# Kernel optimization log

Hardware: AMD Instinct MI355X
Metric: run time of the kernel (lower is better)

Reference implementation:

```python
import jax, jax.numpy as jnp
import numpy as np
from jax import lax

M = 384   # latent_seq_length (match states); insert states = M+1; K = 2M+1
A = 21    # alphabet_length
B = 64    # batch
L = 256   # max observed sequence length
NEG = -1.0e32  # pyro uses -1/epsilon with epsilon=1e-32 for impossible transitions


def _state_indices(Mloc):
    # state k = m + M*g: match states (g=0) m in 0..M-1, insert states (g=1) m in 0..M
    m_k = np.concatenate([np.arange(Mloc), np.arange(Mloc + 1)]).astype(np.int32)
    g_k = np.concatenate([np.zeros(Mloc, np.int32), np.ones(Mloc + 1, np.int32)])
    s_k = (m_k + 1 - g_k).astype(np.int32)  # next decision position, in 0..M
    return m_k, g_k, s_k


def _arrange(precursor_seq_logits, insert_seq_logits, insert_logits, delete_logits):
    """Profile(M) state arranger: assemble initial/transition/emission logits of the
    MuE profile HMM from insertion (r) and deletion (u) log-simplex params.
    insert_logits[m,j] = [log(1-r_mj), log(r_mj)], same for delete/u. Boundary
    convention r_M=1, u_M=0. Vectorized (gathers + cumsum of the delete chain)
    instead of pyro's dense (M,3,2,K,K) transfer einsum -- same math."""
    Mloc = precursor_seq_logits.shape[0]
    dt = precursor_seq_logits.dtype
    m_k, g_k, s_k = _state_indices(Mloc)
    pad_r = jnp.tile(jnp.array([[[NEG, 0.0]]], dt), (1, 3, 1))  # r_M = 1
    pad_u = jnp.tile(jnp.array([[[0.0, NEG]]], dt), (1, 3, 1))  # u_M = 0
    lre = jnp.concatenate([insert_logits, pad_r], 0)  # (M+1,3,2)
    lue = jnp.concatenate([delete_logits, pad_u], 0)  # (M+1,3,2)
    # delete-chain log prob per skipped position j (enter-and-leave delete, type j=2)
    d2 = insert_logits[:, 2, 0] + delete_logits[:, 2, 1]  # (M,)
    C = jnp.concatenate([jnp.zeros((1,), dt), jnp.cumsum(d2), jnp.zeros((1,), dt)])  # C[j]=sum_{i<j} d2[i]
    # per-source-state factors (K,)
    src_stay = lre[s_k, g_k, 0]   # log(1-r_{s,g})
    src_del = lue[s_k, g_k, 1]    # log u_{s,g}
    src_match = lue[s_k, g_k, 0]  # log(1-u_{s,g})
    src_ins = lre[s_k, g_k, 1]    # log r_{s,g}
    # per-target-state factors (K,)
    t_match = lre[m_k, 2, 0] + lue[m_k, 2, 0]
    t_ins = lre[m_k, 2, 1]
    is_ins = g_k == 1
    t_term = jnp.where(is_ins, t_ins, t_match)
    # transition matrix (K,K): direct step, delete-chain step, or impossible
    chain = (src_stay + src_del - C[s_k + 1])[:, None] + C[m_k][None, :]
    same = m_k[None, :] == s_k[:, None]
    fwdm = m_k[None, :] > s_k[:, None]
    direct = jnp.where(is_ins[None, :], src_ins[:, None], (src_stay + src_match)[:, None])
    trans = jnp.where(same, direct, jnp.where(fwdm, chain + t_term[None, :], NEG))
    # initial vector: virtual source (m=-1, g=0) -> s=0 with j=0 params
    i_direct = jnp.where(is_ins, lre[0, 0, 1], lre[0, 0, 0] + lue[0, 0, 0])
    i_chain = lre[0, 0, 0] + lue[0, 0, 1] - C[1] + C[m_k]
    init = jnp.where(m_k == 0, i_direct, i_chain + t_term)
    # emission logits: match states emit precursor, insert states emit insert_seq
    obs = jnp.concatenate([precursor_seq_logits, insert_seq_logits], 0)  # (K,A)
    return init, trans, obs


def _forward(precursor_seq, insert_seq, insert, delete, seq_data, local_scale):
    # log-softmax normalizations done in ProfileHMM.model
    p = precursor_seq - jax.nn.logsumexp(precursor_seq, -1, keepdims=True)
    iseq = insert_seq - jax.nn.logsumexp(insert_seq, -1, keepdims=True)
    r = insert - jax.nn.logsumexp(insert, -1, keepdims=True)
    u = delete - jax.nn.logsumexp(delete, -1, keepdims=True)
    init, trans, obs = _arrange(p, iseq, r, u)
    # MissingDataDiscreteHMM normalizes all logits
    init = init - jax.nn.logsumexp(init)
    trans = trans - jax.nn.logsumexp(trans, -1, keepdims=True)
    obs = obs - jax.nn.logsumexp(obs, -1, keepdims=True)
    # per-position per-state emission log-prob; all-zero rows (missing) give 0
    vl = jnp.einsum('bla,ka->blk', seq_data, obs)  # (B,L,K)
    alpha = init[None, :] + vl[:, 0]               # (B,K)
    Tprob = jnp.exp(trans)                         # (K,K)

    def step(a, vlt):
        # logsumexp_k(a[b,k] + trans[k,kp]) via stable exp-matmul-log
        mx = jnp.max(a, -1, keepdims=True)
        pr = jnp.exp(a - mx) @ Tprob
        return jnp.log(jnp.maximum(pr, 1e-30)) + mx + vlt, None

    alpha, _ = lax.scan(step, alpha, jnp.moveaxis(vl[:, 1:], 1, 0))
    return local_scale[0] * jax.nn.logsumexp(alpha, -1)  # (B,) scaled log-probs


def setup_inputs() -> dict:
    key = jax.random.key(0)
    ks = jax.random.split(key, 6)
    precursor_seq = jax.random.normal(ks[0], (M, A), jnp.float32)
    insert_seq = jax.random.normal(ks[1], (M + 1, A), jnp.float32)
    indel_prior = jnp.array([10.0, 0.0], jnp.float32)  # indel_prior_bias=10 -> rare indels
    insert = indel_prior + jax.random.normal(ks[2], (M, 3, 2), jnp.float32)
    delete = indel_prior + jax.random.normal(ks[3], (M, 3, 2), jnp.float32)
    lengths = jax.random.randint(ks[4], (B,), L // 2, L + 1)
    letters = jax.random.randint(ks[5], (B, L), 0, A)
    onehot = jax.nn.one_hot(letters, A, dtype=jnp.float32)
    mask = (jnp.arange(L)[None, :] < lengths[:, None]).astype(jnp.float32)
    seq_data = onehot * mask[:, :, None]  # zero rows past length = missing data
    return {"precursor_seq": precursor_seq, "insert_seq": insert_seq,
            "insert": insert, "delete": delete, "seq_data": seq_data,
            "local_scale": jnp.ones((1,), jnp.float32)}


def reference(precursor_seq, insert_seq, insert, delete, seq_data, local_scale):
    return _forward(precursor_seq, insert_seq, insert, delete, seq_data, local_scale)
```

## Files before the change

### kernel.cpp

```cpp
#include <hip/hip_runtime.h>


#define NEGC (-1.0e32f)

typedef float v2f __attribute__((ext_vector_type(2)));

#if __has_builtin(__builtin_elementwise_fma)
#define VFMA(a,b,c) __builtin_elementwise_fma((a),(b),(c))
#else
static __device__ __forceinline__ v2f VFMA(v2f a, v2f b, v2f c) {
    v2f r; r.x = fmaf(a.x,b.x,c.x); r.y = fmaf(a.y,b.y,c.y); return r;
}
#endif
#if __has_builtin(__builtin_elementwise_max)
#define VMAX(a,b) __builtin_elementwise_max((a),(b))
#else
static __device__ __forceinline__ v2f VMAX(v2f a, v2f b) {
    v2f r; r.x = fmaxf(a.x,b.x); r.y = fmaxf(a.y,b.y); return r;
}
#endif
static __device__ __forceinline__ v2f mkv2(float a, float b) { v2f r; r.x = a; r.y = b; return r; }

template<int CTRL>
__device__ __forceinline__ float fdpp(float x) {
    union { float f; int i; } u, r;
    u.f = x;
    r.i = __builtin_amdgcn_update_dpp(0, u.i, CTRL, 0xF, 0xF, true);
    return r.f;
}
__device__ __forceinline__ float wsr1(float x) { return fdpp<0x138>(x); }
__device__ __forceinline__ float rdlane63(float x) {
    union { float f; int i; } u; u.f = x;
    u.i = __builtin_amdgcn_readlane(u.i, 63);
    return u.f;
}

#define L_TAB   0
#define L_ES    16128
#define L_LETS  16152
#define L_TOTAL 16224

#define S_RN    0
#define S_UN    2304
#define S_EWS   4608
#define S_ETMM  4993
#define S_ETII  5378
#define S_CS    5763
#define S_QA    6148
#define S_D2    6533
#define S_AEM   6917
#define S_AEI   7302
#define S_DMA   7687
#define S_DMB   8072
#define S_DIA   8457
#define S_DIB   8842
#define S_RAW   9227
#define S_RED   9998

struct Buf { v2f em0, em1, em2, ei0, ei1, ei2; float es; };

#define RENORM do { \
    v2f mv_ = VMAX(VMAX(Pm0,Pm1), VMAX(Pm2, VMAX(Pi0, VMAX(Pi1,Pi2)))); \
    float mxr_ = fmaxf(fmaxf(mv_.x, mv_.y), pi384); \
    mxr_ = fmaxf(mxr_, fdpp<0x111>(mxr_)); \
    mxr_ = fmaxf(mxr_, fdpp<0x112>(mxr_)); \
    mxr_ = fmaxf(mxr_, fdpp<0x114>(mxr_)); \
    mxr_ = fmaxf(mxr_, fdpp<0x118>(mxr_)); \
    mxr_ = fmaxf(mxr_, fdpp<0x142>(mxr_)); \
    mxr_ = fmaxf(mxr_, fdpp<0x143>(mxr_)); \
    float g_ = rdlane63(mxr_); \
    if (g_ > 0.f) { \
        float sc_ = 0x1p60f / g_; \
        logoff += __logf(g_) - 41.588830833596718565f; \
        Pm0 *= sc_; Pm1 *= sc_; Pm2 *= sc_; Pi0 *= sc_; Pi1 *= sc_; Pi2 *= sc_; pi384 *= sc_; \
    } \
} while (0)

#define FILL(LM, E) do { \
    int lmv_ = (LM); \
    int lmc_ = lmv_ > 20 ? 20 : lmv_; \
    const float* bp_ = smem + lmc_*768 + lane12; \
    float4 q0_ = ((const float4*)bp_)[0], q1_ = ((const float4*)bp_)[1], q2_ = ((const float4*)bp_)[2]; \
    E.em0 = mkv2(q0_.x,q0_.y); E.em1 = mkv2(q0_.z,q0_.w); E.em2 = mkv2(q1_.x,q1_.y); \
    E.ei0 = mkv2(q1_.z,q1_.w); E.ei1 = mkv2(q2_.x,q2_.y); E.ei2 = mkv2(q2_.z,q2_.w); \
    E.es = smem[L_ES + lmv_]; \
} while (0)

#define CORE(CUR, FAST) do { \
    float apx_ = wsr1(Pm2.y); \
    float oldPm_ = Pm2.y; \
    v2f Ap0_ = mkv2(apx_, Pm0.x), Ap1_ = mkv2(Pm0.y, Pm1.x), Ap2_ = mkv2(Pm1.y, Pm2.x); \
    v2f E0_ = VFMA(Pi0, Cei0, Ap0_*Cem0); \
    v2f E1_ = VFMA(Pi1, Cei1, Ap1_*Cem1); \
    v2f E2_ = VFMA(Pi2, Cei2, Ap2_*Cem2); \
    float i0_ = E0_.x; \
    float i1_ = fmaf(w1, i0_, E0_.y); \
    float i2_ = fmaf(w2, i1_, E1_.x); \
    float i3_ = fmaf(w3, i2_, E1_.y); \
    float i4_ = fmaf(w4, i3_, E2_.x); \
    float i5_ = fmaf(w5, i4_, E2_.y); \
    float bb_; \
    if (FAST) { bb_ = fmaf(Ar0, wsr1(i5_), i5_); } \
    else { \
        bb_ = i5_; \
        bb_ = fmaf(Ar0, fdpp<0x111>(bb_), bb_); \
        bb_ = fmaf(Ar1, fdpp<0x112>(bb_), bb_); \
        bb_ = fmaf(Ar2, fdpp<0x114>(bb_), bb_); \
        bb_ = fmaf(Ar3, fdpp<0x118>(bb_), bb_); \
        bb_ = fmaf(A15, fdpp<0x142>(bb_), bb_); \
        bb_ = fmaf(A31, fdpp<0x143>(bb_), bb_); \
    } \
    float bx_ = wsr1(bb_); \
    v2f Rv0_ = mkv2(bx_, fmaf(pw1, bx_, i0_)); \
    v2f Rv1_ = mkv2(fmaf(pw2, bx_, i1_), fmaf(pw3, bx_, i2_)); \
    v2f Rv2_ = mkv2(fmaf(pw4, bx_, i3_), fmaf(pw5, bx_, i4_)); \
    v2f nm0_ = VFMA(Cgm0, Rv0_, VFMA(Pi0, Cdmb0, Ap0_*Cdma0)); \
    v2f nm1_ = VFMA(Cgm1, Rv1_, VFMA(Pi1, Cdmb1, Ap1_*Cdma1)); \
    v2f nm2_ = VFMA(Cgm2, Rv2_, VFMA(Pi2, Cdmb2, Ap2_*Cdma2)); \
    v2f ni0_ = VFMA(Cgi0, Rv0_, VFMA(Pi0, Cdib0, Ap0_*Cdia0)); \
    v2f ni1_ = VFMA(Cgi1, Rv1_, VFMA(Pi1, Cdib1, Ap1_*Cdia1)); \
    v2f ni2_ = VFMA(Cgi2, Rv2_, VFMA(Pi2, Cdib2, Ap2_*Cdia2)); \
    float np_ = ((oldPm_ + pi384) + bb_) * CUR.es;  \
    Pm0 = nm0_*CUR.em0; Pm1 = nm1_*CUR.em1; Pm2 = nm2_*CUR.em2; \
    Pi0 = ni0_*CUR.ei0; Pi1 = ni1_*CUR.ei1; Pi2 = ni2_*CUR.ei2; \
    pi384 = np_; \
} while (0)

#define ITER(BA,BB,BC,LA,LB,LC,TIDX,FAST) do { \
    FILL(LA, BC); \
    LA = (int)lets[(TIDX)+5]; \
    CORE(BA, FAST); \
} while (0)

#define SCANLOOP(FAST) do { \
    for (int it = 0; it < bodies; ++it, t += 6) { \
        ITER(bA,bB,bC,lA,lB,lC,t,FAST); \
        ITER(bB,bC,bA,lB,lC,lA,t+1,FAST); \
        ITER(bC,bA,bB,lC,lA,lB,t+2,FAST); \
        ITER(bA,bB,bC,lA,lB,lC,t+3,FAST); \
        ITER(bB,bC,bA,lB,lC,lA,t+4,FAST); \
        ITER(bC,bA,bB,lC,lA,lB,t+5,FAST); \
        RENORM; \
    } \
    if (rem > 0) { ITER(bA,bB,bC,lA,lB,lC,t,FAST); ++t; } \
    if (rem > 1) { ITER(bB,bC,bA,lB,lC,lA,t,FAST); ++t; } \
    if (rem > 2) { ITER(bC,bA,bB,lC,lA,lB,t,FAST); ++t; } \
    if (rem > 3) { ITER(bA,bB,bC,lA,lB,lC,t,FAST); ++t; } \
    if (rem > 4) { ITER(bB,bC,bA,lB,lC,lA,t,FAST); ++t; } \
} while (0)

__global__ __launch_bounds__(256, 1) void hmm_fused(
    const float* __restrict__ ps, const float* __restrict__ iseq,
    const float* __restrict__ rr, const float* __restrict__ uu,
    const float* __restrict__ seq, const float* __restrict__ lsc,
    float* __restrict__ out)
{
    __shared__ float smem[L_TOTAL];
    const int tid = threadIdx.x;
    const int lane = tid & 63;
    const int wvid = tid >> 6;
    const int b = blockIdx.x;
    unsigned char* lets = (unsigned char*)(smem + L_LETS);

    float* rn   = smem + S_RN;
    float* un   = smem + S_UN;
    float* ews  = smem + S_EWS;
    float* etmm = smem + S_ETMM;
    float* etii = smem + S_ETII;
    float* Cs   = smem + S_CS;
    float* qa   = smem + S_QA;
    float* d2s  = smem + S_D2;
    float* cAEM = smem + S_AEM;
    float* cAEI = smem + S_AEI;
    float* cDMA = smem + S_DMA;
    float* cDMB = smem + S_DMB;
    float* cDIA = smem + S_DIA;
    float* cDIB = smem + S_DIB;
    float* rawv = smem + S_RAW;
    float* red  = smem + S_RED;

    {
        const float* p = seq + (size_t)b*5376 + tid*21;
        float s = 0.f, wsum = 0.f;
        #pragma unroll
        for (int a = 0; a < 21; ++a) { float v = p[a]; s += v; wsum += v*(float)a; }
        lets[tid] = (s > 0.5f) ? (unsigned char)(int)(wsum + 0.5f) : (unsigned char)21;
        if (tid < 8) lets[256 + tid] = (unsigned char)21;
    }
    for (int row = tid; row < 1152; row += 256) {
        float a = rr[row*2], c = rr[row*2+1];
        float mx = fmaxf(a, c);
        float l = mx + __logf(__expf(a-mx) + __expf(c-mx));
        rn[row*2] = a - l; rn[row*2+1] = c - l;
        a = uu[row*2]; c = uu[row*2+1];
        mx = fmaxf(a, c);
        l = mx + __logf(__expf(a-mx) + __expf(c-mx));
        un[row*2] = a - l; un[row*2+1] = c - l;
    }
    __syncthreads();
    for (int m = tid; m < 384; m += 256) {
        float d = rn[(m*3+2)*2+0] + un[(m*3+2)*2+1];
        d2s[m] = d;
        ews[m] = __expf(d);
        etmm[m] = __expf(rn[(m*3+2)*2+0] + un[(m*3+2)*2+0]);
        etii[m] = __expf(rn[(m*3+2)*2+1]);
    }
    if (tid == 0) { ews[384] = 0.f; etmm[384] = 0.f; etii[384] = 1.f; }
    __syncthreads();
    if (tid < 64) {
        float incl[6]; float z = 0.f;
        #pragma unroll
        for (int i = 0; i < 6; ++i) { z += d2s[lane*6+i]; incl[i] = z; }
        float tot = z;
        #pragma unroll
        for (int d = 1; d < 64; d <<= 1) { float q = __shfl_up(tot, d); if (lane >= d) tot += q; }
        float excl = __shfl_up(tot, 1); if (lane == 0) excl = 0.f;
        #pragma unroll
        for (int i = 0; i < 6; ++i) Cs[lane*6+i+1] = excl + incl[i];
        if (lane == 0) Cs[0] = 0.f;
    } else if (tid < 128) {
        float wv6[6], xv[6], incl[6];
        #pragma unroll
        for (int i = 0; i < 6; ++i) {
            int s = 384 - (lane*6 + i);
            wv6[i] = ews[s]; xv[i] = etii[s] + etmm[s];
        }
        float z = 0.f, Wl = 1.f;
        #pragma unroll
        for (int i = 0; i < 6; ++i) { z = fmaf(wv6[i], z, xv[i]); incl[i] = z; Wl *= wv6[i]; }
        float val = z, wt = Wl;
        #pragma unroll
        for (int d = 1; d < 64; d <<= 1) {
            float pv = __shfl_up(val, d); float pwv = __shfl_up(wt, d);
            if (lane >= d) { val = fmaf(wt, pv, val); wt *= pwv; }
        }
        float excl = __shfl_up(val, 1); if (lane == 0) excl = 0.f;
        float pp = 1.f;
        #pragma unroll
        for (int i = 0; i < 6; ++i) {
            pp *= wv6[i];
            qa[383 - (lane*6 + i)] = fmaf(excl, pp, incl[i]);
        }
        if (lane == 0) qa[384] = 0.f;
    }
    __syncthreads();
    for (int k = tid; k < 769; k += 256) {
        int g = (k < 384) ? 0 : 1;
        int m = (k < 384) ? k : (k - 384);
        int s = m + 1 - g;
        float ss, sd, smv, si;
        if (s <= 383) {
            int base = (s*3 + g)*2;
            ss = rn[base+0]; si = rn[base+1];
            smv = un[base+0]; sd = un[base+1];
        } else { ss = NEGC; si = 0.f; smv = 0.f; sd = NEGC; }
        float d0 = (s <= 383) ? (ss + smv) : NEGC;
        float d1 = si;
        float q = qa[s];
        float lq = (q > 0.f) ? __logf(q) : -1.0e30f;
        float ch = ss + sd + lq;
        float mx = fmaxf(fmaxf(d0, d1), ch);
        float Z = mx + __logf(__expf(d0-mx) + __expf(d1-mx) + __expf(ch-mx));
        float we = __expf(ss + sd - Z);
        float w0 = __expf(d0 - Z);
        float w1v = __expf(d1 - Z);
        if (g == 0) { cAEM[s] = we; cDMA[s] = w0; cDIA[s] = w1v; }
        else        { cAEI[s] = we; cDMB[s] = w0; cDIB[s] = w1v; }
    }
    if (tid == 0) { cAEM[0] = 0.f; cDMA[0] = 0.f; cDIA[0] = 0.f; }
    {
        float r000 = rn[0], r001 = rn[1];
        float u000 = un[0], u001 = un[1];
        for (int k = tid; k < 769; k += 256) {
            int g = (k < 384) ? 0 : 1;
            int m = (k < 384) ? k : (k - 384);
            float v;
            if (m == 0) v = g ? r001 : (r000 + u000);
            else {
                float tt = g ? ((m <= 383) ? rn[(m*3+2)*2+1] : 0.f)
                             : (rn[(m*3+2)*2+0] + un[(m*3+2)*2+0]);
                v = r000 + u001 - Cs[1] + Cs[m] + tt;
            }
            rawv[k] = v;
        }
    }
    __syncthreads();
    {
        float lmax = -3.0e38f;
        for (int k = tid; k < 769; k += 256) lmax = fmaxf(lmax, rawv[k]);
        #pragma unroll
        for (int d = 1; d < 64; d <<= 1) lmax = fmaxf(lmax, __shfl_xor(lmax, d));
        if (lane == 0) red[wvid] = lmax;
    }
    __syncthreads();
    {
        float gmax = fmaxf(fmaxf(red[0], red[1]), fmaxf(red[2], red[3]));
        float lsum = 0.f;
        for (int k = tid; k < 769; k += 256) lsum += __expf(rawv[k] - gmax);
        #pragma unroll
        for (int d = 1; d < 64; d <<= 1) lsum += __shfl_xor(lsum, d);
        if (lane == 0) red[4 + wvid] = lsum;
        __syncthreads();
        float lse = gmax + __logf(red[4] + red[5] + red[6] + red[7]);
        for (int k = tid; k < 769; k += 256) rawv[k] = __expf(rawv[k] - lse);
    }
    __syncthreads();
    const int j0 = lane*6;
    const int lane12 = lane*12;
    v2f Cem0=mkv2(cAEM[j0],cAEM[j0+1]), Cem1=mkv2(cAEM[j0+2],cAEM[j0+3]), Cem2=mkv2(cAEM[j0+4],cAEM[j0+5]);
    v2f Cei0=mkv2(cAEI[j0],cAEI[j0+1]), Cei1=mkv2(cAEI[j0+2],cAEI[j0+3]), Cei2=mkv2(cAEI[j0+4],cAEI[j0+5]);
    v2f Cdma0=mkv2(cDMA[j0],cDMA[j0+1]), Cdma1=mkv2(cDMA[j0+2],cDMA[j0+3]), Cdma2=mkv2(cDMA[j0+4],cDMA[j0+5]);
    v2f Cdmb0=mkv2(cDMB[j0],cDMB[j0+1]), Cdmb1=mkv2(cDMB[j0+2],cDMB[j0+3]), Cdmb2=mkv2(cDMB[j0+4],cDMB[j0+5]);
    v2f Cdia0=mkv2(cDIA[j0],cDIA[j0+1]), Cdia1=mkv2(cDIA[j0+2],cDIA[j0+3]), Cdia2=mkv2(cDIA[j0+4],cDIA[j0+5]);
    v2f Cdib0=mkv2(cDIB[j0],cDIB[j0+1]), Cdib1=mkv2(cDIB[j0+2],cDIB[j0+3]), Cdib2=mkv2(cDIB[j0+4],cDIB[j0+5]);
    v2f Cgm0=mkv2(etmm[j0],etmm[j0+1]), Cgm1=mkv2(etmm[j0+2],etmm[j0+3]), Cgm2=mkv2(etmm[j0+4],etmm[j0+5]);
    v2f Cgi0=mkv2(etii[j0],etii[j0+1]), Cgi1=mkv2(etii[j0+2],etii[j0+3]), Cgi2=mkv2(etii[j0+4],etii[j0+5]);
    v2f Pm0=mkv2(rawv[j0],rawv[j0+1]), Pm1=mkv2(rawv[j0+2],rawv[j0+3]), Pm2=mkv2(rawv[j0+4],rawv[j0+5]);
    v2f Pi0=mkv2(rawv[384+j0],rawv[384+j0+1]), Pi1=mkv2(rawv[384+j0+2],rawv[384+j0+3]), Pi2=mkv2(rawv[384+j0+4],rawv[384+j0+5]);
    float pi384 = rawv[768];
    const float W0=ews[j0], w1=ews[j0+1], w2=ews[j0+2], w3=ews[j0+3], w4=ews[j0+4], w5=ews[j0+5];
    __syncthreads();
    for (int row = tid; row < 769; row += 256) {
        const float* src = (row < 384) ? (ps + row*21) : (iseq + (row-384)*21);
        float mx = -3.0e38f;
        for (int a = 0; a < 21; ++a) mx = fmaxf(mx, src[a]);
        float sm2 = 0.f;
        for (int a = 0; a < 21; ++a) sm2 += __expf(src[a]-mx);
        float inv = 1.0f / sm2;
        if (row < 768) {
            int j = (row < 384) ? row : (row - 384);
            int slot = (j/6)*12 + ((row < 384) ? 0 : 6) + (j%6);
            float* dst = smem + L_TAB + slot;
            for (int a = 0; a < 21; ++a) dst[a*768] = __expf(src[a]-mx)*inv;
        } else {
            for (int a = 0; a < 21; ++a) smem[L_ES + a] = __expf(src[a]-mx)*inv;
            smem[L_ES + 21] = 1.0f; smem[L_ES + 22] = 1.0f; smem[L_ES + 23] = 1.0f;
        }
    }
    __syncthreads();
    if (wvid != 0) return;

    int n = 0;
    #pragma unroll
    for (int c = 0; c < 4; ++c)
        n += __popcll(__ballot(lets[c*64 + lane] != (unsigned char)21));

    const float pw1 = W0, pw2 = pw1*w1, pw3 = pw2*w2, pw4 = pw3*w3, pw5 = pw4*w4;
    const float W = pw5*w5;
    float p_ = W;
    const float Ar0 = p_;
    { float q = __shfl_up(p_, 1); p_ *= q; } const float Ar1 = p_;
    { float q = __shfl_up(p_, 2); p_ *= q; } const float Ar2 = p_;
    { float q = __shfl_up(p_, 4); p_ *= q; } const float Ar3 = p_;
    float prefR = W;
    #pragma unroll
    for (int d = 1; d < 16; d <<= 1) { float q = __shfl_up(prefR, d); if ((lane & 15) >= d) prefR *= q; }
    const int rw = lane >> 4;
    const float A15 = (rw == 1 || rw == 3) ? prefR : 0.f;
    const float s47 = __shfl(prefR, 47);
    const float A31 = (rw == 2) ? prefR : ((rw == 3) ? prefR * s47 : 0.f);
    bool bad = (Ar1 != 0.f) || (Ar2 != 0.f) || (Ar3 != 0.f)
             || ((A15 != 0.f) && ((lane & 15) >= 1))
             || ((A31 != 0.f) && (lane >= 33));
    const bool fastAll = (__ballot(bad) == 0ull);

    float logoff = 0.f;
    {
        int lm0 = (int)lets[0];
        const float* bp = smem + lm0*768 + lane12;
        float4 q0 = ((const float4*)bp)[0], q1 = ((const float4*)bp)[1], q2 = ((const float4*)bp)[2];
        Pm0 *= mkv2(q0.x,q0.y); Pm1 *= mkv2(q0.z,q0.w); Pm2 *= mkv2(q1.x,q1.y);
        Pi0 *= mkv2(q1.z,q1.w); Pi1 *= mkv2(q2.x,q2.y); Pi2 *= mkv2(q2.z,q2.w);
        pi384 *= smem[L_ES + lm0];
        RENORM;
    }

    Buf bA, bB, bC;
    FILL((int)lets[1], bA);
    FILL((int)lets[2], bB);
    int lA = (int)lets[3], lB = (int)lets[4], lC = (int)lets[5];

    const int total = n - 1;
    const int bodies = total / 6;
    const int rem = total - bodies*6;
    int t = 1;
    if (fastAll) SCANLOOP(1);
    else         SCANLOOP(0);

    v2f sv = Pm0 + Pm1 + Pm2 + Pi0 + Pi1 + Pi2;
    float s = sv.x + sv.y + ((lane == 63) ? pi384 : 0.f);
    s += fdpp<0x111>(s); s += fdpp<0x112>(s); s += fdpp<0x114>(s); s += fdpp<0x118>(s);
    s += fdpp<0x142>(s); s += fdpp<0x143>(s);
    if (lane == 63) out[b] = lsc[0] * (__logf(s) + logoff);
}

extern "C" void kernel_launch(void* const* d_in, const int* in_sizes, int n_in,
                              void* d_out, int out_size, void* d_ws, size_t ws_size,
                              hipStream_t stream)
{
    const float* ps   = (const float*)d_in[0];
    const float* iseq = (const float*)d_in[1];
    const float* ins  = (const float*)d_in[2];
    const float* del  = (const float*)d_in[3];
    const float* seq  = (const float*)d_in[4];
    const float* lsc  = (const float*)d_in[5];
    float* out = (float*)d_out;
    hmm_fused<<<64, 256, 0, stream>>>(ps, iseq, ins, del, seq, lsc, out);
}
```

Baseline: 108.8 us.

## Use power-of-two exponent renormalization, compute shifted carry directly, renormalize every 12 steps

```diff
diff --git a/kernel.cpp b/kernel.cpp
--- a/kernel.cpp
+++ b/kernel.cpp
@@ -21,6 +21,12 @@
 #endif
 static __device__ __forceinline__ v2f mkv2(float a, float b) { v2f r; r.x = a; r.y = b; return r; }
 
+#if __has_builtin(__builtin_amdgcn_sched_barrier)
+#define SCHED_FENCE() __builtin_amdgcn_sched_barrier(0x401)
+#else
+#define SCHED_FENCE()
+#endif
+
 template<int CTRL>
 __device__ __forceinline__ float fdpp(float x) {
     union { float f; int i; } u, r;
@@ -29,11 +35,6 @@
     return r.f;
 }
 __device__ __forceinline__ float wsr1(float x) { return fdpp<0x138>(x); }
-__device__ __forceinline__ float rdlane63(float x) {
-    union { float f; int i; } u; u.f = x;
-    u.i = __builtin_amdgcn_readlane(u.i, 63);
-    return u.f;
-}
 
 #define L_TAB   0
 #define L_ES    16128
@@ -68,12 +69,14 @@
     mxr_ = fmaxf(mxr_, fdpp<0x118>(mxr_)); \
     mxr_ = fmaxf(mxr_, fdpp<0x142>(mxr_)); \
     mxr_ = fmaxf(mxr_, fdpp<0x143>(mxr_)); \
-    float g_ = rdlane63(mxr_); \
-    if (g_ > 0.f) { \
-        float sc_ = 0x1p60f / g_; \
-        logoff += __logf(g_) - 41.588830833596718565f; \
-        Pm0 *= sc_; Pm1 *= sc_; Pm2 *= sc_; Pi0 *= sc_; Pi1 *= sc_; Pi2 *= sc_; pi384 *= sc_; \
-    } \
+    union { float f; int i; } ub_; ub_.f = mxr_; \
+    int bits_ = __builtin_amdgcn_readlane(ub_.i, 63); \
+    int E_ = (bits_ >> 23) & 0xff; \
+    E_ = (E_ < 71) ? 71 : E_; \
+    ksum += 197 - E_; \
+    union { int i; float f; } us_; us_.i = (324 - E_) << 23; \
+    float sc_ = us_.f; \
+    Pm0 *= sc_; Pm1 *= sc_; Pm2 *= sc_; Pi0 *= sc_; Pi1 *= sc_; Pi2 *= sc_; pi384 *= sc_; \
 } while (0)
 
 #define FILL(LM, E) do { \
@@ -99,9 +102,12 @@
     float i3_ = fmaf(w3, i2_, E1_.y); \
     float i4_ = fmaf(w4, i3_, E2_.x); \
     float i5_ = fmaf(w5, i4_, E2_.y); \
-    float bb_; \
-    if (FAST) { bb_ = fmaf(Ar0, wsr1(i5_), i5_); } \
-    else { \
+    float bb_, bx_; \
+    if (FAST) { \
+        float u_ = wsr1(i5_); \
+        bb_ = fmaf(Ar0, u_, i5_);              \
+        bx_ = fmaf(Ar0s, wsr1(u_), u_);        \
+    } else { \
         bb_ = i5_; \
         bb_ = fmaf(Ar0, fdpp<0x111>(bb_), bb_); \
         bb_ = fmaf(Ar1, fdpp<0x112>(bb_), bb_); \
@@ -109,8 +115,8 @@
         bb_ = fmaf(Ar3, fdpp<0x118>(bb_), bb_); \
         bb_ = fmaf(A15, fdpp<0x142>(bb_), bb_); \
         bb_ = fmaf(A31, fdpp<0x143>(bb_), bb_); \
+        bx_ = wsr1(bb_); \
     } \
-    float bx_ = wsr1(bb_); \
     v2f Rv0_ = mkv2(bx_, fmaf(pw1, bx_, i0_)); \
     v2f Rv1_ = mkv2(fmaf(pw2, bx_, i1_), fmaf(pw3, bx_, i2_)); \
     v2f Rv2_ = mkv2(fmaf(pw4, bx_, i3_), fmaf(pw5, bx_, i4_)); \
@@ -130,23 +136,36 @@
     FILL(LA, BC); \
     LA = (int)lets[(TIDX)+5]; \
     CORE(BA, FAST); \
+    SCHED_FENCE(); \
 } while (0)
 
 #define SCANLOOP(FAST) do { \
-    for (int it = 0; it < bodies; ++it, t += 6) { \
+    for (int it = 0; it < bodies; ++it, t += 12) { \
         ITER(bA,bB,bC,lA,lB,lC,t,FAST); \
         ITER(bB,bC,bA,lB,lC,lA,t+1,FAST); \
         ITER(bC,bA,bB,lC,lA,lB,t+2,FAST); \
         ITER(bA,bB,bC,lA,lB,lC,t+3,FAST); \
         ITER(bB,bC,bA,lB,lC,lA,t+4,FAST); \
         ITER(bC,bA,bB,lC,lA,lB,t+5,FAST); \
+        ITER(bA,bB,bC,lA,lB,lC,t+6,FAST); \
+        ITER(bB,bC,bA,lB,lC,lA,t+7,FAST); \
+        ITER(bC,bA,bB,lC,lA,lB,t+8,FAST); \
+        ITER(bA,bB,bC,lA,lB,lC,t+9,FAST); \
+        ITER(bB,bC,bA,lB,lC,lA,t+10,FAST); \
+        ITER(bC,bA,bB,lC,lA,lB,t+11,FAST); \
         RENORM; \
     } \
-    if (rem > 0) { ITER(bA,bB,bC,lA,lB,lC,t,FAST); ++t; } \
-    if (rem > 1) { ITER(bB,bC,bA,lB,lC,lA,t,FAST); ++t; } \
-    if (rem > 2) { ITER(bC,bA,bB,lC,lA,lB,t,FAST); ++t; } \
-    if (rem > 3) { ITER(bA,bB,bC,lA,lB,lC,t,FAST); ++t; } \
-    if (rem > 4) { ITER(bB,bC,bA,lB,lC,lA,t,FAST); ++t; } \
+    if (rem > 0)  { ITER(bA,bB,bC,lA,lB,lC,t,FAST); ++t; } \
+    if (rem > 1)  { ITER(bB,bC,bA,lB,lC,lA,t,FAST); ++t; } \
+    if (rem > 2)  { ITER(bC,bA,bB,lC,lA,lB,t,FAST); ++t; } \
+    if (rem > 3)  { ITER(bA,bB,bC,lA,lB,lC,t,FAST); ++t; } \
+    if (rem > 4)  { ITER(bB,bC,bA,lB,lC,lA,t,FAST); ++t; } \
+    if (rem > 5)  { ITER(bC,bA,bB,lC,lA,lB,t,FAST); ++t; } \
+    if (rem > 6)  { ITER(bA,bB,bC,lA,lB,lC,t,FAST); ++t; } \
+    if (rem > 7)  { ITER(bB,bC,bA,lB,lC,lA,t,FAST); ++t; } \
+    if (rem > 8)  { ITER(bC,bA,bB,lC,lA,lB,t,FAST); ++t; } \
+    if (rem > 9)  { ITER(bA,bB,bC,lA,lB,lC,t,FAST); ++t; } \
+    if (rem > 10) { ITER(bB,bC,bA,lB,lC,lA,t,FAST); ++t; } \
 } while (0)
 
 __global__ __launch_bounds__(256, 1) void hmm_fused(
@@ -349,6 +368,7 @@
     const float W = pw5*w5;
     float p_ = W;
     const float Ar0 = p_;
+    const float Ar0s = wsr1(Ar0);
     { float q = __shfl_up(p_, 1); p_ *= q; } const float Ar1 = p_;
     { float q = __shfl_up(p_, 2); p_ *= q; } const float Ar2 = p_;
     { float q = __shfl_up(p_, 4); p_ *= q; } const float Ar3 = p_;
@@ -364,7 +384,7 @@
              || ((A31 != 0.f) && (lane >= 33));
     const bool fastAll = (__ballot(bad) == 0ull);
 
-    float logoff = 0.f;
+    int ksum = 0;
     {
         int lm0 = (int)lets[0];
         const float* bp = smem + lm0*768 + lane12;
@@ -381,8 +401,8 @@
     int lA = (int)lets[3], lB = (int)lets[4], lC = (int)lets[5];
 
     const int total = n - 1;
-    const int bodies = total / 6;
-    const int rem = total - bodies*6;
+    const int bodies = total / 12;
+    const int rem = total - bodies*12;
     int t = 1;
     if (fastAll) SCANLOOP(1);
     else         SCANLOOP(0);
@@ -391,7 +411,7 @@
     float s = sv.x + sv.y + ((lane == 63) ? pi384 : 0.f);
     s += fdpp<0x111>(s); s += fdpp<0x112>(s); s += fdpp<0x114>(s); s += fdpp<0x118>(s);
     s += fdpp<0x142>(s); s += fdpp<0x143>(s);
-    if (lane == 63) out[b] = lsc[0] * (__logf(s) + logoff);
+    if (lane == 63) out[b] = lsc[0] * (__logf(s) - (float)ksum * 0.69314718055994531f);
 }
 
 extern "C" void kernel_launch(void* const* d_in, const int* in_sizes, int n_in,
```

After: 106.1 us. -2.5%, faster.
